# Optimization experiments

Measured on AMD Instinct MI355X. Metric: run time of the kernel, lower is better.

## Reference

```python
import jax, jax.numpy as jnp
import numpy as np

T_MAX = 0.5
LN_EPS = 1e-5
B, N, D = 256, 16384, 512
NNZ = N * 33  # ~ (2*top_k+1) nonzeros per row of the sparse Laplacian
DF = 4 * D
DT = 32  # time-embedding hidden size


def _layernorm(x, g, b):
    mu = jnp.mean(x, axis=-1, keepdims=True)
    var = jnp.mean((x - mu) ** 2, axis=-1, keepdims=True)
    return (x - mu) * jax.lax.rsqrt(var + LN_EPS) * g + b


def setup_inputs() -> dict:
    key = jax.random.key(0)
    ks = jax.random.split(key, 16)

    def lin_w(k, fan_out, fan_in):
        return jax.random.normal(k, (fan_out, fan_in), jnp.float32) * (1.0 / np.sqrt(fan_in))

    inp = {}
    inp["x0"] = jax.random.uniform(ks[0], (B, N), jnp.float32)
    inp["t"] = jax.random.uniform(ks[1], (B,), jnp.float32)
    inp["L_vals"] = jax.random.normal(ks[2], (NNZ,), jnp.float32) * 0.1
    inp["W_in"] = lin_w(ks[3], D, N)
    inp["b_in"] = jnp.zeros((D,), jnp.float32)
    inp["W_out"] = lin_w(ks[4], N, D)
    inp["b_out"] = jnp.zeros((N,), jnp.float32)
    inp["W_qkv"] = lin_w(ks[5], 3 * D, D)
    inp["b_qkv"] = jnp.zeros((3 * D,), jnp.float32)
    inp["W_o"] = lin_w(ks[6], D, D)
    inp["b_o"] = jnp.zeros((D,), jnp.float32)
    inp["g1"] = jnp.ones((D,), jnp.float32)
    inp["be1"] = jnp.zeros((D,), jnp.float32)
    inp["g2"] = jnp.ones((D,), jnp.float32)
    inp["be2"] = jnp.zeros((D,), jnp.float32)
    inp["W_f1"] = lin_w(ks[7], DF, D)
    inp["b_f1"] = jnp.zeros((DF,), jnp.float32)
    inp["W_f2"] = lin_w(ks[8], D, DF)
    inp["b_f2"] = jnp.zeros((D,), jnp.float32)
    inp["W_t1"] = lin_w(ks[9], DT, 1)
    inp["b_t1"] = jnp.zeros((DT,), jnp.float32)
    inp["W_t2"] = lin_w(ks[10], D, DT)
    inp["b_t2"] = jnp.zeros((D,), jnp.float32)
    inp["L_rows"] = jax.random.randint(ks[11], (NNZ,), 0, N, jnp.int32)
    inp["L_cols"] = jax.random.randint(ks[12], (NNZ,), 0, N, jnp.int32)
    return inp


def reference(x0, t, L_vals, W_in, b_in, W_out, b_out, W_qkv, b_qkv, W_o, b_o,
              g1, be1, g2, be2, W_f1, b_f1, W_f2, b_f2, W_t1, b_t1, W_t2, b_t2,
              L_rows, L_cols):
    n_items = x0.shape[1]
    d_model = W_in.shape[0]
    t_cont = t * T_MAX  # per-sample diffusion time (explicit input, not RNG)

    # Batched sparse Laplacian diffusion (replaces the per-row torch.sparse.mm loop):
    # (L @ x.T)[i, b] = sum_e L_vals[e] * x0[b, L_cols[e]] aggregated to row L_rows[e]
    contrib = x0[:, L_cols] * L_vals                                  # (B, NNZ)
    Lx = jax.ops.segment_sum(contrib.T, L_rows, num_segments=n_items)  # (N, B)
    x_t = x0 - t_cont[:, None] * Lx.T                                  # (B, N)

    # Denoiser (eval mode: dropout off)
    h = x_t @ W_in.T + b_in                                            # (B, D)
    t_norm = t_cont / T_MAX
    te = jax.nn.silu(t_norm[:, None] @ W_t1.T + b_t1) @ W_t2.T + b_t2  # (B, D)
    h = h + te

    # MultiheadAttention on a length-1 sequence: softmax over one key is exactly 1,
    # so attn_out = out_proj(V) with V = h @ W_v.T + b_v.
    qkv = h @ W_qkv.T + b_qkv                                          # (B, 3D)
    v = qkv[:, 2 * d_model:]
    attn_out = v @ W_o.T + b_o

    h = _layernorm(h + attn_out, g1, be1)
    ff = jax.nn.gelu(h @ W_f1.T + b_f1, approximate=False) @ W_f2.T + b_f2
    h = _layernorm(h + ff, g2, be2)

    pred = h @ W_out.T + b_out                                         # (B, N)
    return jnp.mean((pred - x0) ** 2)
```

## Files before the change

### kernel.cpp

```cpp
#include <hip/hip_runtime.h>
#include <math.h>

#define Bb   256
#define Nn   16384
#define Dd   512
#define NNZn 540672
#define DFf  2048
#define SLOT 128

#define CVT_BLKS 2560
#define TR_BLKS  1024
#define BK_BLKS  2112

typedef __bf16 bf16;
typedef __bf16 bf16x4 __attribute__((ext_vector_type(4)));
typedef __bf16 bf16x8 __attribute__((ext_vector_type(8)));
typedef float  f32x4  __attribute__((ext_vector_type(4)));

__device__ __forceinline__ void gload16(const void* g, void* l) {
  __builtin_amdgcn_global_load_lds(
      (const __attribute__((address_space(1))) unsigned int*)g,
      (__attribute__((address_space(3))) unsigned int*)l, 16, 0, 0);
}

__global__ __launch_bounds__(256) void k_prep(
    const float* __restrict__ w_v, const float* __restrict__ w_o,
    const float* __restrict__ w_f1, const float* __restrict__ w_f2,
    bf16* __restrict__ o_v, bf16* __restrict__ o_o,
    bf16* __restrict__ o_f1, bf16* __restrict__ o_f2,
    const float* __restrict__ x0, bf16* __restrict__ x0T,
    const int* __restrict__ rows, const int* __restrict__ cols,
    const float* __restrict__ vals,
    int* __restrict__ counts, int2* __restrict__ ents) {
  __shared__ float tile[64][65];
  int blk = blockIdx.x;
  if (blk < CVT_BLKS) {
    int v = blk * 256 + threadIdx.x;
    const float* s; bf16* d; int base;
    if (v < 131072) {
      if (v < 65536) { s = w_v;  d = o_v;  base = 0; }
      else           { s = w_o;  d = o_o;  base = 65536; }
    } else {
      if (v < 393216) { s = w_f1; d = o_f1; base = 131072; }
      else            { s = w_f2; d = o_f2; base = 393216; }
    }
    int idx = (v - base) * 4;
    float4 x = *(const float4*)(s + idx);
    bf16x4 o;
    o[0] = (bf16)x.x; o[1] = (bf16)x.y; o[2] = (bf16)x.z; o[3] = (bf16)x.w;
    *(bf16x4*)(d + idx) = o;
  } else if (blk < CVT_BLKS + TR_BLKS) {
    int bx = blk - CVT_BLKS;
    int n0 = (bx & 255) * 64, b0 = (bx >> 8) * 64;
    int tx = threadIdx.x & 63, ty = threadIdx.x >> 6;
#pragma unroll
    for (int i = 0; i < 16; i++) {
      int bl = ty * 16 + i;
      tile[bl][tx] = x0[(size_t)(b0 + bl) * Nn + n0 + tx];
    }
    __syncthreads();
#pragma unroll
    for (int i = 0; i < 16; i++) {
      int nl = ty * 16 + i;
      x0T[(size_t)(n0 + nl) * Bb + b0 + tx] = (bf16)tile[tx][nl];
    }
  } else {
    int i = (blk - CVT_BLKS - TR_BLKS) * 256 + threadIdx.x;
    int r = rows[i];
    int p = atomicAdd(&counts[r], 1);
    if (p < SLOT)
      ents[(size_t)r * SLOT + p] = make_int2(cols[i], __float_as_int(vals[i]));
  }
}

__global__ __launch_bounds__(256) void k_lx(const bf16x4* __restrict__ x0T4,
                                            const int* __restrict__ counts,
                                            const int2* __restrict__ ents,
                                            bf16x4* __restrict__ Lx4) {
  int w = threadIdx.x >> 6, lane = threadIdx.x & 63;
  int r = blockIdx.x * 4 + w;
  __shared__ int2 esm[4][64];
  int cnt = counts[r];
  const int2* ep = ents + (size_t)r * SLOT;
  float a0 = 0.f, a1 = 0.f, a2 = 0.f, a3 = 0.f;
  float b0 = 0.f, b1 = 0.f, b2 = 0.f, b3 = 0.f;
  for (int base = 0; base < cnt; base += 64) {
    int m = cnt - base; if (m > 64) m = 64;
    if (lane < m) esm[w][lane] = ep[base + lane];
    int i = 0;
    for (; i + 1 < m; i += 2) {
      int2 e0 = esm[w][i], e1 = esm[w][i + 1];
      bf16x4 xv0 = x0T4[(size_t)e0.x * 64 + lane];
      bf16x4 xv1 = x0T4[(size_t)e1.x * 64 + lane];
      float v0 = __int_as_float(e0.y), v1 = __int_as_float(e1.y);
      a0 += v0 * (float)xv0[0]; a1 += v0 * (float)xv0[1];
      a2 += v0 * (float)xv0[2]; a3 += v0 * (float)xv0[3];
      b0 += v1 * (float)xv1[0]; b1 += v1 * (float)xv1[1];
      b2 += v1 * (float)xv1[2]; b3 += v1 * (float)xv1[3];
    }
    if (i < m) {
      int2 e0 = esm[w][i];
      bf16x4 xv0 = x0T4[(size_t)e0.x * 64 + lane];
      float v0 = __int_as_float(e0.y);
      a0 += v0 * (float)xv0[0]; a1 += v0 * (float)xv0[1];
      a2 += v0 * (float)xv0[2]; a3 += v0 * (float)xv0[3];
    }
  }
  bf16x4 o;
  o[0] = (bf16)(a0 + b0); o[1] = (bf16)(a1 + b1);
  o[2] = (bf16)(a2 + b2); o[3] = (bf16)(a3 + b3);
  Lx4[(size_t)r * 64 + lane] = o;
}

__global__ __launch_bounds__(256) void k_combine(const float* __restrict__ x0,
                                                 const bf16* __restrict__ Lx,
                                                 const float* __restrict__ t,
                                                 bf16* __restrict__ xt) {
  __shared__ float lxs[64][65];
  int n0 = blockIdx.x * 64, b0 = blockIdx.y * 64;
  int tx = threadIdx.x & 63, ty = threadIdx.x >> 6;
#pragma unroll
  for (int i = 0; i < 16; i++) {
    int nl = ty * 16 + i;
    lxs[nl][tx] = (float)Lx[(size_t)(n0 + nl) * Bb + b0 + tx];
  }
  __syncthreads();
#pragma unroll
  for (int i = 0; i < 16; i++) {
    int bl = ty * 16 + i;
    int b  = b0 + bl;
    float tc = t[b] * 0.5f;
    float v = x0[(size_t)b * Nn + n0 + tx] - tc * lxs[tx][bl];
    xt[(size_t)b * Nn + n0 + tx] = (bf16)v;
  }
}

template <int BM, int BN, int MODE, int ACT = 0, int BF32 = 0>
__global__ __launch_bounds__(256) void gemm_tn(
    const bf16* __restrict__ A, const void* __restrict__ Bmv,
    float* __restrict__ C, int N, int K, int kLen, int MN,
    const float* __restrict__ bias, const float* __restrict__ x0,
    float* __restrict__ lossOut) {
  constexpr int WM = BM / 2, WN = BN / 2, FM = WM / 16, FN = WN / 16;
  constexpr int PA = (BM * 64) / 4096, PB = (BN * 64) / 4096;
  __shared__ __align__(16) bf16 As[BM * 32];
  __shared__ __align__(16) bf16 Bs[BN * 32];
  const int tid = threadIdx.x;
  const int lane = tid & 63, w = tid >> 6;
  const int wm = w >> 1, wn = w & 1;
  const int mBase = blockIdx.x * BM, nBase = blockIdx.y * BN;
  const int k0 = blockIdx.z * kLen;

  f32x4 acc[FM][FN];
#pragma unroll
  for (int i = 0; i < FM; i++)
#pragma unroll
    for (int j = 0; j < FN; j++) acc[i][j] = {0.f, 0.f, 0.f, 0.f};

  for (int kk = 0; kk < kLen; kk += 32) {
    const int k = k0 + kk;
    __syncthreads();
#pragma unroll
    for (int p = 0; p < PA; p++) {
      int u = p * 256 + tid;
      gload16(A + (size_t)(mBase + (u >> 2)) * K + k + (u & 3) * 8,
              (char*)As + p * 4096 + w * 1024);
    }
    if constexpr (BF32) {
      const float* Bf = (const float*)Bmv;
#pragma unroll
      for (int p = 0; p < BN * 32 / 1024; p++) {
        int u = p * 256 + tid;
        int row = u >> 3, sub = u & 7;
        float4 x = *(const float4*)(Bf + (size_t)(nBase + row) * K + k + sub * 4);
        bf16x4 o;
        o[0] = (bf16)x.x; o[1] = (bf16)x.y; o[2] = (bf16)x.z; o[3] = (bf16)x.w;
        *(bf16x4*)(Bs + row * 32 + sub * 4) = o;
      }
    } else {
      const bf16* Bm = (const bf16*)Bmv;
#pragma unroll
      for (int p = 0; p < PB; p++) {
        int u = p * 256 + tid;
        gload16(Bm + (size_t)(nBase + (u >> 2)) * K + k + (u & 3) * 8,
                (char*)Bs + p * 4096 + w * 1024);
      }
    }
    __syncthreads();
    bf16x8 af[FM], bfr[FN];
#pragma unroll
    for (int i = 0; i < FM; i++)
      af[i] = *(const bf16x8*)(As + (wm * WM + i * 16 + (lane & 15)) * 32 + (lane >> 4) * 8);
#pragma unroll
    for (int j = 0; j < FN; j++)
      bfr[j] = *(const bf16x8*)(Bs + (wn * WN + j * 16 + (lane & 15)) * 32 + (lane >> 4) * 8);
#pragma unroll
    for (int i = 0; i < FM; i++)
#pragma unroll
      for (int j = 0; j < FN; j++)
        acc[i][j] = __builtin_amdgcn_mfma_f32_16x16x32_bf16(af[i], bfr[j], acc[i][j], 0, 0, 0);
  }

  if constexpr (MODE == 0) {
    float* Cz = C + (size_t)blockIdx.z * MN;
#pragma unroll
    for (int i = 0; i < FM; i++)
#pragma unroll
      for (int j = 0; j < FN; j++) {
        int n  = nBase + wn * WN + j * 16 + (lane & 15);
        int mB = mBase + wm * WM + i * 16 + ((lane >> 4) << 2);
#pragma unroll
        for (int r = 0; r < 4; r++)
          Cz[(size_t)(mB + r) * N + n] = acc[i][j][r];
      }
  } else if constexpr (MODE == 1) {
    bf16* Cb = (bf16*)C;
#pragma unroll
    for (int i = 0; i < FM; i++)
#pragma unroll
      for (int j = 0; j < FN; j++) {
        int n  = nBase + wn * WN + j * 16 + (lane & 15);
        float bo = bias[n];
        int mB = mBase + wm * WM + i * 16 + ((lane >> 4) << 2);
#pragma unroll
        for (int r = 0; r < 4; r++) {
          float x = acc[i][j][r] + bo;
          if constexpr (ACT == 1)
            x = 0.5f * x * (1.f + erff(x * 0.70710678118654752f));
          Cb[(size_t)(mB + r) * N + n] = (bf16)x;
        }
      }
  } else {
    float lsum = 0.f;
#pragma unroll
    for (int i = 0; i < FM; i++)
#pragma unroll
      for (int j = 0; j < FN; j++) {
        int n  = nBase + wn * WN + j * 16 + (lane & 15);
        float bo = bias[n];
        int mB = mBase + wm * WM + i * 16 + ((lane >> 4) << 2);
#pragma unroll
        for (int r = 0; r < 4; r++) {
          float d = acc[i][j][r] + bo - x0[(size_t)(mB + r) * N + n];
          lsum += d * d;
        }
      }
    for (int off = 32; off > 0; off >>= 1) lsum += __shfl_down(lsum, off, 64);
    if (lane == 0) atomicAdd(lossOut, lsum);
  }
}

__global__ __launch_bounds__(512) void k_epi_h(const float* __restrict__ P,
                                               const float* __restrict__ t,
                                               const float* __restrict__ W_t1,
                                               const float* __restrict__ b_t1,
                                               const float* __restrict__ W_t2,
                                               const float* __restrict__ b_t2,
                                               const float* __restrict__ b_in,
                                               float* __restrict__ h_f32,
                                               bf16* __restrict__ h_b) {
  int b = blockIdx.x, d = threadIdx.x;
  __shared__ float s[32];
  if (d < 32) {
    float z = t[b] * W_t1[d] + b_t1[d];
    s[d] = z / (1.f + expf(-z));
  }
  __syncthreads();
  int i = b * Dd + d;
  float v = b_in[d] + b_t2[d];
#pragma unroll
  for (int sp = 0; sp < 32; sp++) v += P[sp * (Bb * Dd) + i];
#pragma unroll
  for (int j = 0; j < 32; j++) v += s[j] * W_t2[d * 32 + j];
  h_f32[i] = v;
  h_b[i] = (bf16)v;
}

template <int NS>
__global__ __launch_bounds__(512) void k_ln(const float* __restrict__ base,
                                            const float* __restrict__ add,
                                            const float* __restrict__ bias,
                                            const float* __restrict__ g,
                                            const float* __restrict__ be,
                                            float* __restrict__ out_f32,
                                            bf16* __restrict__ out_b) {
  int b = blockIdx.x, d = threadIdx.x;
  __shared__ float red[16];
  int i = b * Dd + d;
  float x = base[i] + bias[d];
#pragma unroll
  for (int sp = 0; sp < NS; sp++) x += add[sp * (Bb * Dd) + i];
  int w = d >> 6, lane = d & 63;
  float s = x;
  for (int off = 32; off > 0; off >>= 1) s += __shfl_down(s, off, 64);
  if (lane == 0) red[w] = s;
  __syncthreads();
  if (d == 0) {
    float tot = 0.f;
    for (int q = 0; q < 8; q++) tot += red[q];
    red[8] = tot * (1.f / 512.f);
  }
  __syncthreads();
  float mu = red[8];
  float c = x - mu;
  float s2 = c * c;
  for (int off = 32; off > 0; off >>= 1) s2 += __shfl_down(s2, off, 64);
  if (lane == 0) red[w] = s2;
  __syncthreads();
  if (d == 0) {
    float tot = 0.f;
    for (int q = 0; q < 8; q++) tot += red[q];
    red[8] = tot * (1.f / 512.f);
  }
  __syncthreads();
  float var = red[8];
  float y = c * rsqrtf(var + 1e-5f) * g[d] + be[d];
  if (out_f32) out_f32[i] = y;
  out_b[i] = (bf16)y;
}

__global__ void k_final(const float* __restrict__ loss, float* __restrict__ out) {
  if (threadIdx.x == 0 && blockIdx.x == 0)
    out[0] = loss[0] * (1.f / 4194304.f);
}

extern "C" void kernel_launch(void* const* d_in, const int* in_sizes, int n_in,
                              void* d_out, int out_size, void* d_ws, size_t ws_size,
                              hipStream_t stream) {
  const float* x0    = (const float*)d_in[0];
  const float* t     = (const float*)d_in[1];
  const float* Lv    = (const float*)d_in[2];
  const float* W_in  = (const float*)d_in[3];
  const float* b_in  = (const float*)d_in[4];
  const float* W_out = (const float*)d_in[5];
  const float* b_out = (const float*)d_in[6];
  const float* W_qkv = (const float*)d_in[7];
  const float* b_qkv = (const float*)d_in[8];
  const float* W_o   = (const float*)d_in[9];
  const float* b_o   = (const float*)d_in[10];
  const float* g1    = (const float*)d_in[11];
  const float* be1   = (const float*)d_in[12];
  const float* g2    = (const float*)d_in[13];
  const float* be2   = (const float*)d_in[14];
  const float* W_f1  = (const float*)d_in[15];
  const float* b_f1  = (const float*)d_in[16];
  const float* W_f2  = (const float*)d_in[17];
  const float* b_f2  = (const float*)d_in[18];
  const float* W_t1  = (const float*)d_in[19];
  const float* b_t1  = (const float*)d_in[20];
  const float* W_t2  = (const float*)d_in[21];
  const float* b_t2  = (const float*)d_in[22];
  const int* L_rows  = (const int*)d_in[23];
  const int* L_cols  = (const int*)d_in[24];

  size_t off = 0;
  char* ws = (char*)d_ws;
  auto carve = [&](size_t bytes) -> void* {
    void* p = ws + off;
    off += (bytes + 255) & ~(size_t)255;
    return p;
  };

  bf16* W_v_b    = (bf16*)carve((size_t)Dd * Dd * 2);
  bf16* W_o_b    = (bf16*)carve((size_t)Dd * Dd * 2);
  bf16* W_f1_b   = (bf16*)carve((size_t)DFf * Dd * 2);
  bf16* W_f2_b   = (bf16*)carve((size_t)Dd * DFf * 2);
  bf16* x0T_b    = (bf16*)carve((size_t)Nn * Bb * 2);
  bf16* Lx_b     = (bf16*)carve((size_t)Nn * Bb * 2);
  bf16* xt_b     = (bf16*)carve((size_t)Bb * Nn * 2);
  float* p_h     = (float*)carve((size_t)32 * Bb * Dd * 4);
  float* p_at    = (float*)carve((size_t)Bb * Dd * 4);
  float* p_f2    = (float*)carve((size_t)4 * Bb * Dd * 4);
  float* h_f32   = (float*)carve((size_t)Bb * Dd * 4);
  bf16* h_b      = (bf16*)carve((size_t)Bb * Dd * 2);
  bf16* v_b      = (bf16*)carve((size_t)Bb * Dd * 2);
  float* hln_f32 = (float*)carve((size_t)Bb * Dd * 4);
  bf16* hln_b    = (bf16*)carve((size_t)Bb * Dd * 2);
  bf16* f1_b     = (bf16*)carve((size_t)Bb * DFf * 2);
  bf16* h2_b     = (bf16*)carve((size_t)Bb * Dd * 2);
  int* counts    = (int*)carve((size_t)Nn * 4);
  float* lossw   = (float*)carve(256);
  int2* ents     = (int2*)carve((size_t)Nn * SLOT * 8);
  (void)in_sizes; (void)n_in; (void)out_size; (void)ws_size; (void)Lv;

  hipMemsetAsync(counts, 0, (size_t)Nn * 4 + 256, stream);

  k_prep<<<CVT_BLKS + TR_BLKS + BK_BLKS, 256, 0, stream>>>(
      W_qkv + (size_t)2 * Dd * Dd, W_o, W_f1, W_f2,
      W_v_b, W_o_b, W_f1_b, W_f2_b,
      x0, x0T_b, L_rows, L_cols, Lv, counts, ents);

  k_lx<<<Nn / 4, 256, 0, stream>>>((const bf16x4*)x0T_b, counts, ents,
                                   (bf16x4*)Lx_b);
  k_combine<<<dim3(256, 4), 256, 0, stream>>>(x0, Lx_b, t, xt_b);

  gemm_tn<128, 128, 0, 0, 1><<<dim3(2, 4, 32), 256, 0, stream>>>(
      xt_b, W_in, p_h, Dd, Nn, 512, Bb * Dd, nullptr, nullptr, nullptr);
  k_epi_h<<<Bb, 512, 0, stream>>>(p_h, t, W_t1, b_t1, W_t2, b_t2, b_in, h_f32, h_b);

  gemm_tn<64, 64, 1><<<dim3(4, 8, 1), 256, 0, stream>>>(
      h_b, W_v_b, (float*)v_b, Dd, Dd, 512, 0, b_qkv + 2 * Dd, nullptr, nullptr);

  gemm_tn<64, 64, 0><<<dim3(4, 8, 1), 256, 0, stream>>>(
      v_b, W_o_b, p_at, Dd, Dd, 512, 0, nullptr, nullptr, nullptr);
  k_ln<1><<<Bb, 512, 0, stream>>>(h_f32, p_at, b_o, g1, be1, hln_f32, hln_b);

  gemm_tn<64, 64, 1, 1><<<dim3(4, 32, 1), 256, 0, stream>>>(
      hln_b, W_f1_b, (float*)f1_b, DFf, Dd, 512, 0, b_f1, nullptr, nullptr);

  gemm_tn<64, 64, 0><<<dim3(4, 8, 4), 256, 0, stream>>>(
      f1_b, W_f2_b, p_f2, Dd, DFf, 512, Bb * Dd, nullptr, nullptr, nullptr);
  k_ln<4><<<Bb, 512, 0, stream>>>(hln_f32, p_f2, b_f2, g2, be2, nullptr, h2_b);

  gemm_tn<128, 128, 2, 0, 1><<<dim3(2, 128, 1), 256, 0, stream>>>(
      h2_b, W_out, nullptr, Nn, Dd, 512, 0, b_out, x0, lossw);
  k_final<<<1, 64, 0, stream>>>(lossw, (float*)d_out);
}
```

Before: 330.9 us.

## Triple-buffer GEMM loads, pre-convert big weights, pack sparse entries, shrink tiles

The GEMM kernel now uses a three-stage LDS ring with vmcnt-based partial waits, so global-to-LDS loads overlap MFMA compute instead of syncing on every k step. W_in and W_out are converted to bf16 in the prep kernel, which removes the in-loop fp32 B path. Sparse entries are packed into 32 bits (16-bit column plus fp16 value) with the slot count halved. Tile sizes are reduced to launch more blocks, and the loss reduction does one atomic per block instead of one per wave. In exchange, the 16-bit column field only holds indices below 65536, fp16 values lose precision, rows with more than 64 entries are truncated, and the prep kernel now does extra full weight conversions every call.

```diff
diff --git a/kernel.cpp b/kernel.cpp
--- a/kernel.cpp
+++ b/kernel.cpp
@@ -6,11 +6,18 @@
 #define Dd   512
 #define NNZn 540672
 #define DFf  2048
-#define SLOT 128
-
-#define CVT_BLKS 2560
+#define SLOT 64
+
+#define CVT_BLKS 4736
 #define TR_BLKS  1024
 #define BK_BLKS  2112
+
+#define C1 65536
+#define C2 131072
+#define C3 393216
+#define C4 655360
+#define C5 2752512
+#define C6 4849664
 
 typedef __bf16 bf16;
 typedef __bf16 bf16x4 __attribute__((ext_vector_type(4)));
@@ -23,32 +30,43 @@
       (__attribute__((address_space(3))) unsigned int*)l, 16, 0, 0);
 }
 
+template <int NK>
+__device__ __forceinline__ void bar_keep() {
+  asm volatile("s_waitcnt vmcnt(%0) lgkmcnt(0)" :: "n"(NK) : "memory");
+  __builtin_amdgcn_s_barrier();
+}
+
 __global__ __launch_bounds__(256) void k_prep(
     const float* __restrict__ w_v, const float* __restrict__ w_o,
     const float* __restrict__ w_f1, const float* __restrict__ w_f2,
+    const float* __restrict__ w_in, const float* __restrict__ w_out,
     bf16* __restrict__ o_v, bf16* __restrict__ o_o,
     bf16* __restrict__ o_f1, bf16* __restrict__ o_f2,
+    bf16* __restrict__ o_in, bf16* __restrict__ o_out,
     const float* __restrict__ x0, bf16* __restrict__ x0T,
     const int* __restrict__ rows, const int* __restrict__ cols,
     const float* __restrict__ vals,
-    int* __restrict__ counts, int2* __restrict__ ents) {
+    int* __restrict__ counts, unsigned* __restrict__ ents) {
   __shared__ float tile[64][65];
   int blk = blockIdx.x;
   if (blk < CVT_BLKS) {
-    int v = blk * 256 + threadIdx.x;
-    const float* s; bf16* d; int base;
-    if (v < 131072) {
-      if (v < 65536) { s = w_v;  d = o_v;  base = 0; }
-      else           { s = w_o;  d = o_o;  base = 65536; }
-    } else {
-      if (v < 393216) { s = w_f1; d = o_f1; base = 131072; }
-      else            { s = w_f2; d = o_f2; base = 393216; }
-    }
-    int idx = (v - base) * 4;
-    float4 x = *(const float4*)(s + idx);
-    bf16x4 o;
-    o[0] = (bf16)x.x; o[1] = (bf16)x.y; o[2] = (bf16)x.z; o[3] = (bf16)x.w;
-    *(bf16x4*)(d + idx) = o;
+    int v0i = blk * 1024 + threadIdx.x;
+#pragma unroll
+    for (int j = 0; j < 4; j++) {
+      int v = v0i + j * 256;
+      const float* s; bf16* d; int base;
+      if (v < C2)      { if (v < C1) { s = w_v;  d = o_v;  base = 0;  }
+                         else        { s = w_o;  d = o_o;  base = C1; } }
+      else if (v < C4) { if (v < C3) { s = w_f1; d = o_f1; base = C2; }
+                         else        { s = w_f2; d = o_f2; base = C3; } }
+      else             { if (v < C5) { s = w_in; d = o_in; base = C4; }
+                         else        { s = w_out; d = o_out; base = C5; } }
+      int idx = (v - base) * 4;
+      float4 x = *(const float4*)(s + idx);
+      bf16x4 o;
+      o[0] = (bf16)x.x; o[1] = (bf16)x.y; o[2] = (bf16)x.z; o[3] = (bf16)x.w;
+      *(bf16x4*)(d + idx) = o;
+    }
   } else if (blk < CVT_BLKS + TR_BLKS) {
     int bx = blk - CVT_BLKS;
     int n0 = (bx & 255) * 64, b0 = (bx >> 8) * 64;
@@ -68,20 +86,25 @@
     int i = (blk - CVT_BLKS - TR_BLKS) * 256 + threadIdx.x;
     int r = rows[i];
     int p = atomicAdd(&counts[r], 1);
-    if (p < SLOT)
-      ents[(size_t)r * SLOT + p] = make_int2(cols[i], __float_as_int(vals[i]));
+    if (p < SLOT) {
+      _Float16 hv = (_Float16)vals[i];
+      unsigned short us;
+      __builtin_memcpy(&us, &hv, 2);
+      ents[(size_t)r * SLOT + p] = ((unsigned)cols[i] << 16) | (unsigned)us;
+    }
   }
 }
 
 __global__ __launch_bounds__(256) void k_lx(const bf16x4* __restrict__ x0T4,
                                             const int* __restrict__ counts,
-                                            const int2* __restrict__ ents,
+                                            const unsigned* __restrict__ ents,
                                             bf16x4* __restrict__ Lx4) {
   int w = threadIdx.x >> 6, lane = threadIdx.x & 63;
   int r = blockIdx.x * 4 + w;
-  __shared__ int2 esm[4][64];
+  __shared__ unsigned esm[4][64];
   int cnt = counts[r];
-  const int2* ep = ents + (size_t)r * SLOT;
+  if (cnt > SLOT) cnt = SLOT;
+  const unsigned* ep = ents + (size_t)r * SLOT;
   float a0 = 0.f, a1 = 0.f, a2 = 0.f, a3 = 0.f;
   float b0 = 0.f, b1 = 0.f, b2 = 0.f, b3 = 0.f;
   for (int base = 0; base < cnt; base += 64) {
@@ -89,19 +112,27 @@
     if (lane < m) esm[w][lane] = ep[base + lane];
     int i = 0;
     for (; i + 1 < m; i += 2) {
-      int2 e0 = esm[w][i], e1 = esm[w][i + 1];
-      bf16x4 xv0 = x0T4[(size_t)e0.x * 64 + lane];
-      bf16x4 xv1 = x0T4[(size_t)e1.x * 64 + lane];
-      float v0 = __int_as_float(e0.y), v1 = __int_as_float(e1.y);
+      unsigned e0 = esm[w][i], e1 = esm[w][i + 1];
+      bf16x4 xv0 = x0T4[(size_t)(e0 >> 16) * 64 + lane];
+      bf16x4 xv1 = x0T4[(size_t)(e1 >> 16) * 64 + lane];
+      unsigned short u0 = (unsigned short)(e0 & 0xffff);
+      unsigned short u1 = (unsigned short)(e1 & 0xffff);
+      _Float16 h0, h1;
+      __builtin_memcpy(&h0, &u0, 2);
+      __builtin_memcpy(&h1, &u1, 2);
+      float v0 = (float)h0, v1 = (float)h1;
       a0 += v0 * (float)xv0[0]; a1 += v0 * (float)xv0[1];
       a2 += v0 * (float)xv0[2]; a3 += v0 * (float)xv0[3];
       b0 += v1 * (float)xv1[0]; b1 += v1 * (float)xv1[1];
       b2 += v1 * (float)xv1[2]; b3 += v1 * (float)xv1[3];
     }
     if (i < m) {
-      int2 e0 = esm[w][i];
-      bf16x4 xv0 = x0T4[(size_t)e0.x * 64 + lane];
-      float v0 = __int_as_float(e0.y);
+      unsigned e0 = esm[w][i];
+      bf16x4 xv0 = x0T4[(size_t)(e0 >> 16) * 64 + lane];
+      unsigned short u0 = (unsigned short)(e0 & 0xffff);
+      _Float16 h0;
+      __builtin_memcpy(&h0, &u0, 2);
+      float v0 = (float)h0;
       a0 += v0 * (float)xv0[0]; a1 += v0 * (float)xv0[1];
       a2 += v0 * (float)xv0[2]; a3 += v0 * (float)xv0[3];
     }
@@ -135,21 +166,24 @@
   }
 }
 
-template <int BM, int BN, int MODE, int ACT = 0, int BF32 = 0>
+template <int BM, int BN, int MODE, int ACT = 0>
 __global__ __launch_bounds__(256) void gemm_tn(
-    const bf16* __restrict__ A, const void* __restrict__ Bmv,
+    const bf16* __restrict__ A, const bf16* __restrict__ Bm,
     float* __restrict__ C, int N, int K, int kLen, int MN,
     const float* __restrict__ bias, const float* __restrict__ x0,
     float* __restrict__ lossOut) {
   constexpr int WM = BM / 2, WN = BN / 2, FM = WM / 16, FN = WN / 16;
-  constexpr int PA = (BM * 64) / 4096, PB = (BN * 64) / 4096;
-  __shared__ __align__(16) bf16 As[BM * 32];
-  __shared__ __align__(16) bf16 Bs[BN * 32];
+  constexpr int PASS = (BM + BN) / 64;
+  constexpr int KEEP = PASS;
+  __shared__ __align__(16) bf16 As[3][BM * 32];
+  __shared__ __align__(16) bf16 Bs[3][BN * 32];
+  __shared__ float lred[4];
   const int tid = threadIdx.x;
   const int lane = tid & 63, w = tid >> 6;
   const int wm = w >> 1, wn = w & 1;
   const int mBase = blockIdx.x * BM, nBase = blockIdx.y * BN;
   const int k0 = blockIdx.z * kLen;
+  const int nIter = kLen >> 5;
 
   f32x4 acc[FM][FN];
 #pragma unroll
@@ -157,48 +191,61 @@
 #pragma unroll
     for (int j = 0; j < FN; j++) acc[i][j] = {0.f, 0.f, 0.f, 0.f};
 
-  for (int kk = 0; kk < kLen; kk += 32) {
-    const int k = k0 + kk;
-    __syncthreads();
-#pragma unroll
-    for (int p = 0; p < PA; p++) {
-      int u = p * 256 + tid;
-      gload16(A + (size_t)(mBase + (u >> 2)) * K + k + (u & 3) * 8,
-              (char*)As + p * 4096 + w * 1024);
-    }
-    if constexpr (BF32) {
-      const float* Bf = (const float*)Bmv;
-#pragma unroll
-      for (int p = 0; p < BN * 32 / 1024; p++) {
-        int u = p * 256 + tid;
-        int row = u >> 3, sub = u & 7;
-        float4 x = *(const float4*)(Bf + (size_t)(nBase + row) * K + k + sub * 4);
-        bf16x4 o;
-        o[0] = (bf16)x.x; o[1] = (bf16)x.y; o[2] = (bf16)x.z; o[3] = (bf16)x.w;
-        *(bf16x4*)(Bs + row * 32 + sub * 4) = o;
+  auto stage = [&](int buf, int k) {
+#pragma unroll
+    for (int p = 0; p < PASS; p++) {
+      int c = p * 4 + w;
+      int u = c * 64 + lane;
+      if (c < BM / 16) {
+        int row = u >> 2, sub = u & 3;
+        gload16(A + (size_t)(mBase + row) * K + k + sub * 8,
+                (char*)As[buf] + c * 1024);
+      } else {
+        int u2 = u - BM * 4;
+        int row = u2 >> 2, sub = u2 & 3;
+        gload16(Bm + (size_t)(nBase + row) * K + k + sub * 8,
+                (char*)Bs[buf] + (c - BM / 16) * 1024);
       }
-    } else {
-      const bf16* Bm = (const bf16*)Bmv;
-#pragma unroll
-      for (int p = 0; p < PB; p++) {
-        int u = p * 256 + tid;
-        gload16(Bm + (size_t)(nBase + (u >> 2)) * K + k + (u & 3) * 8,
-                (char*)Bs + p * 4096 + w * 1024);
-      }
-    }
-    __syncthreads();
+    }
+  };
+  auto compute = [&](int cur) {
     bf16x8 af[FM], bfr[FN];
 #pragma unroll
     for (int i = 0; i < FM; i++)
-      af[i] = *(const bf16x8*)(As + (wm * WM + i * 16 + (lane & 15)) * 32 + (lane >> 4) * 8);
+      af[i] = *(const bf16x8*)(As[cur] + (wm * WM + i * 16 + (lane & 15)) * 32 + (lane >> 4) * 8);
 #pragma unroll
     for (int j = 0; j < FN; j++)
-      bfr[j] = *(const bf16x8*)(Bs + (wn * WN + j * 16 + (lane & 15)) * 32 + (lane >> 4) * 8);
+      bfr[j] = *(const bf16x8*)(Bs[cur] + (wn * WN + j * 16 + (lane & 15)) * 32 + (lane >> 4) * 8);
 #pragma unroll
     for (int i = 0; i < FM; i++)
 #pragma unroll
       for (int j = 0; j < FN; j++)
         acc[i][j] = __builtin_amdgcn_mfma_f32_16x16x32_bf16(af[i], bfr[j], acc[i][j], 0, 0, 0);
+  };
+
+  stage(0, k0);
+  if (nIter > 1) {
+    stage(1, k0 + 32);
+    bar_keep<KEEP>();
+  } else {
+    bar_keep<0>();
+  }
+
+  int c0 = 0, c1 = 1, c2 = 2;
+  for (int t = 0; t < nIter; t += 2) {
+    {
+      const bool more2 = (t + 2 < nIter);
+      if (more2) stage(c2, k0 + (t + 2) * 32);
+      compute(c0);
+      if (more2) bar_keep<KEEP>(); else bar_keep<0>();
+    }
+    {
+      const bool more2 = (t + 3 < nIter);
+      if (more2) stage(c0, k0 + (t + 3) * 32);
+      compute(c1);
+      if (more2) bar_keep<KEEP>(); else bar_keep<0>();
+    }
+    int tmp = c2; c2 = c1; c1 = c0; c0 = tmp;
   }
 
   if constexpr (MODE == 0) {
@@ -246,7 +293,10 @@
         }
       }
     for (int off = 32; off > 0; off >>= 1) lsum += __shfl_down(lsum, off, 64);
-    if (lane == 0) atomicAdd(lossOut, lsum);
+    if (lane == 0) lred[w] = lsum;
+    __syncthreads();
+    if (tid == 0)
+      atomicAdd(lossOut, lred[0] + lred[1] + lred[2] + lred[3]);
   }
 }
 
@@ -365,6 +415,8 @@
   bf16* W_o_b    = (bf16*)carve((size_t)Dd * Dd * 2);
   bf16* W_f1_b   = (bf16*)carve((size_t)DFf * Dd * 2);
   bf16* W_f2_b   = (bf16*)carve((size_t)Dd * DFf * 2);
+  bf16* W_in_b   = (bf16*)carve((size_t)Dd * Nn * 2);
+  bf16* W_out_b  = (bf16*)carve((size_t)Nn * Dd * 2);
   bf16* x0T_b    = (bf16*)carve((size_t)Nn * Bb * 2);
   bf16* Lx_b     = (bf16*)carve((size_t)Nn * Bb * 2);
   bf16* xt_b     = (bf16*)carve((size_t)Bb * Nn * 2);
@@ -380,39 +432,39 @@
   bf16* h2_b     = (bf16*)carve((size_t)Bb * Dd * 2);
   int* counts    = (int*)carve((size_t)Nn * 4);
   float* lossw   = (float*)carve(256);
-  int2* ents     = (int2*)carve((size_t)Nn * SLOT * 8);
+  unsigned* ents = (unsigned*)carve((size_t)Nn * SLOT * 4);
   (void)in_sizes; (void)n_in; (void)out_size; (void)ws_size; (void)Lv;
 
   hipMemsetAsync(counts, 0, (size_t)Nn * 4 + 256, stream);
 
   k_prep<<<CVT_BLKS + TR_BLKS + BK_BLKS, 256, 0, stream>>>(
-      W_qkv + (size_t)2 * Dd * Dd, W_o, W_f1, W_f2,
-      W_v_b, W_o_b, W_f1_b, W_f2_b,
+      W_qkv + (size_t)2 * Dd * Dd, W_o, W_f1, W_f2, W_in, W_out,
+      W_v_b, W_o_b, W_f1_b, W_f2_b, W_in_b, W_out_b,
       x0, x0T_b, L_rows, L_cols, Lv, counts, ents);
 
   k_lx<<<Nn / 4, 256, 0, stream>>>((const bf16x4*)x0T_b, counts, ents,
                                    (bf16x4*)Lx_b);
   k_combine<<<dim3(256, 4), 256, 0, stream>>>(x0, Lx_b, t, xt_b);
 
-  gemm_tn<128, 128, 0, 0, 1><<<dim3(2, 4, 32), 256, 0, stream>>>(
-      xt_b, W_in, p_h, Dd, Nn, 512, Bb * Dd, nullptr, nullptr, nullptr);
+  gemm_tn<64, 64, 0><<<dim3(4, 8, 32), 256, 0, stream>>>(
+      xt_b, W_in_b, p_h, Dd, Nn, 512, Bb * Dd, nullptr, nullptr, nullptr);
   k_epi_h<<<Bb, 512, 0, stream>>>(p_h, t, W_t1, b_t1, W_t2, b_t2, b_in, h_f32, h_b);
 
-  gemm_tn<64, 64, 1><<<dim3(4, 8, 1), 256, 0, stream>>>(
+  gemm_tn<32, 32, 1><<<dim3(8, 16, 1), 256, 0, stream>>>(
       h_b, W_v_b, (float*)v_b, Dd, Dd, 512, 0, b_qkv + 2 * Dd, nullptr, nullptr);
 
-  gemm_tn<64, 64, 0><<<dim3(4, 8, 1), 256, 0, stream>>>(
+  gemm_tn<32, 32, 0><<<dim3(8, 16, 1), 256, 0, stream>>>(
       v_b, W_o_b, p_at, Dd, Dd, 512, 0, nullptr, nullptr, nullptr);
   k_ln<1><<<Bb, 512, 0, stream>>>(h_f32, p_at, b_o, g1, be1, hln_f32, hln_b);
 
-  gemm_tn<64, 64, 1, 1><<<dim3(4, 32, 1), 256, 0, stream>>>(
+  gemm_tn<32, 32, 1, 1><<<dim3(8, 64, 1), 256, 0, stream>>>(
       hln_b, W_f1_b, (float*)f1_b, DFf, Dd, 512, 0, b_f1, nullptr, nullptr);
 
-  gemm_tn<64, 64, 0><<<dim3(4, 8, 4), 256, 0, stream>>>(
+  gemm_tn<32, 32, 0><<<dim3(8, 16, 4), 256, 0, stream>>>(
       f1_b, W_f2_b, p_f2, Dd, DFf, 512, Bb * Dd, nullptr, nullptr, nullptr);
   k_ln<4><<<Bb, 512, 0, stream>>>(hln_f32, p_f2, b_f2, g2, be2, nullptr, h2_b);
 
-  gemm_tn<128, 128, 2, 0, 1><<<dim3(2, 128, 1), 256, 0, stream>>>(
-      h2_b, W_out, nullptr, Nn, Dd, 512, 0, b_out, x0, lossw);
+  gemm_tn<64, 64, 2><<<dim3(4, 256, 1), 256, 0, stream>>>(
+      h2_b, W_out_b, nullptr, Nn, Dd, 512, 0, b_out, x0, lossw);
   k_final<<<1, 64, 0, stream>>>(lossw, (float*)d_out);
 }
```

After: 309.5 us. 6.5% less time.
